# Optimization experiments

Measured on AMD Instinct MI355X. Metric: run time of the kernel, lower is better.

Reference implementation:

```python
import jax, jax.numpy as jnp
import numpy as np

N_HEADS = 12
WINDOW = 12
STRIDE = 3
N_ANCHORS = 12
EPS = 1e-6


def fmap(x):
    # elu(x) + 1 non-negative feature map
    return jax.nn.elu(x) + 1.0


def setup_inputs() -> dict:
    key = jax.random.key(0)
    ks = jax.random.split(key, 4)
    B, S, D = 4, 2048, 768
    x = jax.random.normal(ks[0], (B, S, D), dtype=jnp.float32)
    qkv_w = jax.random.normal(ks[1], (3 * D, D), dtype=jnp.float32) * 0.02
    out_w = jax.random.normal(ks[2], (D, D), dtype=jnp.float32) * 0.02
    anchor_q = jax.random.normal(ks[3], (1, N_ANCHORS, D), dtype=jnp.float32) * 0.02
    w_local = jnp.float32(1.0 / 2.0)
    w_stride = jnp.float32(1.0 / 3.0)
    w_global = jnp.float32(1.0 / 6.0)
    return {"x": x, "qkv_w": qkv_w, "out_w": out_w, "anchor_q": anchor_q,
            "w_local": w_local, "w_stride": w_stride, "w_global": w_global}


def _local_band(q, k, v, window):
    B, H, S, D = q.shape
    w = min(window, S)
    half = w // 2
    # pad with zeros BEFORE feature map (padded keys become elu(0)+1 = 1, as in torch)
    k_pad = jnp.pad(k, ((0, 0), (0, 0), (half, half), (0, 0)))
    v_pad = jnp.pad(v, ((0, 0), (0, 0), (half, half), (0, 0)))
    q_f = fmap(q)
    k_f = fmap(k_pad)
    idx = jnp.arange(S)[:, None] + jnp.arange(w)[None, :]  # [S, w] window gather
    k_unf = k_f[:, :, idx, :]   # [B,H,S,w,D]
    v_unf = v_pad[:, :, idx, :]  # [B,H,S,w,D]
    qk = jnp.einsum('bhsd,bhswd->bhsw', q_f, k_unf)
    out = jnp.einsum('bhsw,bhswd->bhsd', qk, v_unf)
    norm = jnp.clip(qk.sum(-1, keepdims=True), 1e-6, None)
    return out / norm


def _stride_band(q, k, v, stride):
    k_s = fmap(k[:, :, ::stride])
    v_s = v[:, :, ::stride]
    q_f = fmap(q)
    kv = jnp.einsum('bhsd,bhse->bhde', k_s, v_s)
    out = jnp.einsum('bhsd,bhde->bhse', q_f, kv)
    k_sum = k_s.sum(axis=2)
    norm = jnp.clip(jnp.einsum('bhsd,bhd->bhs', q_f, k_sum)[..., None], 1e-6, None)
    return out / norm


def _global_band(q, k, v, anchor_q, n_heads, n_anchors):
    B, H, S, D = q.shape
    aq = anchor_q.reshape(1, n_heads, n_anchors, D)  # [1,H,A,hd]
    aq = jnp.broadcast_to(aq, (B, n_heads, n_anchors, D))
    aq_f = fmap(aq)
    k_f = fmap(k)
    kv = jnp.einsum('bhsd,bhse->bhde', k_f, v)
    anchor_out = jnp.einsum('bhad,bhde->bhae', aq_f, kv)
    k_sum = k_f.sum(axis=2)
    anchor_norm = jnp.clip(jnp.einsum('bhad,bhd->bha', aq_f, k_sum)[..., None], 1e-6, None)
    anchor_out = anchor_out / anchor_norm
    q_f = fmap(q)
    anchor_k = fmap(aq)
    qk = jnp.einsum('bhsd,bhad->bhsa', q_f, anchor_k)
    out = jnp.einsum('bhsa,bhae->bhse', qk, anchor_out)
    qk_sum = jnp.clip(qk.sum(-1, keepdims=True), 1e-6, None)
    return out / qk_sum


def reference(x, qkv_w, out_w, anchor_q, w_local, w_stride, w_global):
    B, S, D = x.shape
    H = N_HEADS
    hd = D // H
    qkv = (x @ qkv_w.T).reshape(B, S, 3, H, hd)
    qkv = jnp.transpose(qkv, (2, 0, 3, 1, 4))  # [3,B,H,S,hd]
    q, k, v = qkv[0], qkv[1], qkv[2]
    wn = jax.nn.softmax(jnp.stack([w_local, w_stride, w_global]))
    wl, ws, wg = wn[0], wn[1], wn[2]
    out_local = _local_band(q, k, v, WINDOW)
    out_stride = _stride_band(q, k, v, STRIDE)
    out_global = _global_band(q, k, v, anchor_q, H, N_ANCHORS)
    out = wl * out_local + ws * out_stride + wg * out_global
    out = jnp.transpose(out, (0, 2, 1, 3)).reshape(B, S, D)
    return out @ out_w.T
```

## Files before the change

### kernel.cpp

```cpp
#include <hip/hip_runtime.h>
#include <hip/hip_bf16.h>

#define B_ 4
#define S_ 2048
#define D_ 768
#define H_ 12
#define HD 64

typedef __attribute__((ext_vector_type(8))) short short8;
typedef __attribute__((ext_vector_type(4))) float f32x4;

__device__ __forceinline__ float fmapf(float x) { return x > 0.f ? x + 1.f : __expf(x); }

__device__ __forceinline__ unsigned short f2bu(float f) {
    unsigned u = __float_as_uint(f);
    u += 0x7FFFu + ((u >> 16) & 1u);
    return (unsigned short)(u >> 16);
}
__device__ __forceinline__ float bu2f(unsigned short v) {
    return __uint_as_float((unsigned)v << 16);
}

__device__ __forceinline__ void gload16(const void* g, void* l) {
    __builtin_amdgcn_global_load_lds((__attribute__((address_space(1))) void*)(size_t)g,
                                     (__attribute__((address_space(3))) void*)l, 16, 0, 0);
}

union u16x8 {
    uint4 u;
    short8 s;
    unsigned short h[8];
};

__global__ __launch_bounds__(256) void convert_all(const float* __restrict__ x,
                                                   const float* __restrict__ qkvw,
                                                   const float* __restrict__ outw,
                                                   const float* __restrict__ aq,
                                                   unsigned short* __restrict__ xb,
                                                   unsigned short* __restrict__ wb,
                                                   unsigned short* __restrict__ outwb,
                                                   unsigned short* __restrict__ aqfb_g) {
    int gid = blockIdx.x * 256 + threadIdx.x;
    const float* src;
    unsigned short* dst;
    int i4;
    if (gid < 1572864) {
        src = x; dst = xb; i4 = gid;
    } else if (gid < 1572864 + 442368) {
        src = qkvw; dst = wb; i4 = gid - 1572864;
    } else if (gid < 2162688) {
        src = outw; dst = outwb; i4 = gid - (1572864 + 442368);
    } else {
        int i = gid - 2162688;
        aqfb_g[i] = f2bu(fmapf(aq[i]));
        return;
    }
    float4 v = *(const float4*)&src[i4 * 4];
    ushort4 o;
    o.x = f2bu(v.x); o.y = f2bu(v.y); o.z = f2bu(v.z); o.w = f2bu(v.w);
    *(ushort4*)&dst[i4 * 4] = o;
}

__global__ __launch_bounds__(256) void qkv_gemm_mfma(const unsigned short* __restrict__ xb,
                                                     const unsigned short* __restrict__ wb,
                                                     unsigned short* __restrict__ qfb,
                                                     unsigned short* __restrict__ kfb,
                                                     unsigned short* __restrict__ vvb) {
    __shared__ __attribute__((aligned(16))) unsigned short shmem[18432];
    const int K = 768;
    int orig = blockIdx.x;
    int swz = (orig & 7) * 144 + (orig >> 3);
    int mt = swz / 18, nt = swz - mt * 18;
    int n0 = nt * 128, m0 = mt * 128;
    int tid = threadIdx.x, lane = tid & 63, wave = tid >> 6;
    int wm = (wave & 1) * 64, wn = (wave >> 1) * 64;
    int quad = lane >> 4, l15 = lane & 15;
    f32x4 acc[4][4];
#pragma unroll
    for (int i = 0; i < 4; i++)
#pragma unroll
        for (int j = 0; j < 4; j++) acc[i][j] = 0.f;

    const unsigned short* ga0 = xb + (size_t)(m0 + (tid >> 2)) * K + (tid & 3) * 8;
    const unsigned short* ga1 = xb + (size_t)(m0 + 64 + (tid >> 2)) * K + (tid & 3) * 8;
    const unsigned short* gb0 = wb + (size_t)(n0 + (tid >> 2)) * K + (tid & 3) * 8;
    const unsigned short* gb1 = wb + (size_t)(n0 + 64 + (tid >> 2)) * K + (tid & 3) * 8;

    auto stage = [&](int bufi, int kk) {
        gload16(ga0 + kk, shmem + bufi * 4096 + wave * 512);
        gload16(ga1 + kk, shmem + bufi * 4096 + 2048 + wave * 512);
        gload16(gb0 + kk, shmem + 8192 + bufi * 4096 + wave * 512);
        gload16(gb1 + kk, shmem + 8192 + bufi * 4096 + 2048 + wave * 512);
    };
    auto compute = [&](int bufi) {
        short8 af[4], bfr[4];
#pragma unroll
        for (int i = 0; i < 4; i++)
            af[i] = *(short8*)&shmem[bufi * 4096 + (wm + i * 16 + l15) * 32 + quad * 8];
#pragma unroll
        for (int j = 0; j < 4; j++)
            bfr[j] = *(short8*)&shmem[8192 + bufi * 4096 + (wn + j * 16 + l15) * 32 + quad * 8];
#pragma unroll
        for (int i = 0; i < 4; i++)
#pragma unroll
            for (int j = 0; j < 4; j++)
                acc[i][j] = __builtin_amdgcn_mfma_f32_16x16x32_bf16(af[i], bfr[j], acc[i][j], 0, 0, 0);
    };

    stage(0, 0);
    int buf = 0;
    for (int t = 0; t < 23; t++) {
        stage(buf ^ 1, (t + 1) * 32);
        asm volatile("s_waitcnt vmcnt(4)" ::: "memory");
        __builtin_amdgcn_s_barrier();
        __builtin_amdgcn_sched_barrier(0);
        compute(buf);
        asm volatile("" ::: "memory");
        __builtin_amdgcn_s_barrier();
        buf ^= 1;
    }
    asm volatile("s_waitcnt vmcnt(0)" ::: "memory");
    __builtin_amdgcn_s_barrier();
    __builtin_amdgcn_sched_barrier(0);
    compute(buf);

    __syncthreads();
    {
        int colbase = n0 + wn;
        int t3 = colbase / 768;
        int r = colbase - t3 * 768;
        int h = r >> 6;
        int mstart = m0 + wm;
        int bb = mstart >> 11, sstart = mstart & 2047;
        unsigned short* ldsw = shmem + wave * 4608;
#pragma unroll
        for (int j = 0; j < 4; j++)
#pragma unroll
            for (int i = 0; i < 4; i++)
#pragma unroll
                for (int rr = 0; rr < 4; rr++) {
                    float val = acc[i][j][rr];
                    unsigned short o = (t3 == 2) ? f2bu(val) : f2bu(fmapf(val));
                    ldsw[(i * 16 + quad * 4 + rr) * 72 + j * 16 + l15] = o;
                }
        unsigned short* gb = (t3 == 0 ? qfb : (t3 == 1 ? kfb : vvb)) +
                             (((size_t)(bb * H_ + h) * S_) + sstart) * (size_t)HD;
#pragma unroll
        for (int c = 0; c < 8; c++) {
            int tok = c * 8 + (lane >> 3);
            uint4 vd = *(uint4*)&ldsw[tok * 72 + (lane & 7) * 8];
            *(uint4*)&gb[(size_t)tok * 64 + (lane & 7) * 8] = vd;
        }
    }
}

__global__ __launch_bounds__(512) void band_partial(const unsigned short* __restrict__ kfb,
                                                    const unsigned short* __restrict__ vvb,
                                                    float* __restrict__ pkv,
                                                    float* __restrict__ pks) {
    int bh = blockIdx.x >> 4, chunk = blockIdx.x & 15;
    int sbase = chunk * 128;
    const unsigned short* kfp = kfb + (size_t)bh * S_ * HD + (size_t)sbase * HD;
    const unsigned short* vp = vvb + (size_t)bh * S_ * HD + (size_t)sbase * HD;
    int tid = threadIdx.x;
    int d = tid & 63, eg = tid >> 6, e0 = eg * 8;
    float accg[8], accs[8];
#pragma unroll
    for (int i = 0; i < 8; i++) { accg[i] = 0.f; accs[i] = 0.f; }
    float ksg = 0.f, kss = 0.f;
#pragma unroll 4
    for (int s = 0; s < 128; s++) {
        float kd = bu2f(kfp[(size_t)s * HD + d]);
        bool str = ((sbase + s) % 3) == 0;
        ksg += kd;
        u16x8 va;
        va.u = *(const uint4*)&vp[(size_t)s * HD + e0];
        float vf[8];
#pragma unroll
        for (int i = 0; i < 8; i++) vf[i] = bu2f(va.h[i]);
#pragma unroll
        for (int i = 0; i < 8; i++) accg[i] += kd * vf[i];
        if (str) {
            kss += kd;
#pragma unroll
            for (int i = 0; i < 8; i++) accs[i] += kd * vf[i];
        }
    }
    float* pg = pkv + (size_t)blockIdx.x * 2 * 4096;
#pragma unroll
    for (int i = 0; i < 8; i++) pg[d * 64 + e0 + i] = accg[i];
#pragma unroll
    for (int i = 0; i < 8; i++) pg[4096 + d * 64 + e0 + i] = accs[i];
    if (eg == 0) {
        pks[blockIdx.x * 128 + d] = ksg;
        pks[blockIdx.x * 128 + 64 + d] = kss;
    }
}

__global__ __launch_bounds__(256) void band_reduce(const float* __restrict__ pkv,
                                                   const float* __restrict__ pks,
                                                   const float* __restrict__ aq,
                                                   unsigned short* __restrict__ kvsTb,
                                                   unsigned short* __restrict__ ksumsb,
                                                   unsigned short* __restrict__ aoutTb) {
    int bh = blockIdx.x >> 2, eb = blockIdx.x & 3, e0 = eb * 16;
    int h = bh % H_;
    __shared__ float kvgL[64][17];
    __shared__ float ksgL[64];
    __shared__ float anorm[12];
    int tid = threadIdx.x;
    for (int idx = tid; idx < 1024; idx += 256) {
        int d = idx >> 4, j = idx & 15;
        float sg = 0.f, ss = 0.f;
        const float* p = pkv + (size_t)(bh * 16) * 2 * 4096 + d * 64 + e0 + j;
#pragma unroll 4
        for (int c = 0; c < 16; c++) {
            sg += p[0];
            ss += p[4096];
            p += 2 * 4096;
        }
        kvgL[d][j] = sg;
        kvsTb[(size_t)bh * 4096 + (e0 + j) * 64 + d] = f2bu(ss);
    }
    if (tid < 64) {
        float sg = 0.f, ss = 0.f;
#pragma unroll 4
        for (int c = 0; c < 16; c++) {
            sg += pks[(bh * 16 + c) * 128 + tid];
            ss += pks[(bh * 16 + c) * 128 + 64 + tid];
        }
        ksgL[tid] = sg;
        if (eb == 0) ksumsb[bh * 64 + tid] = f2bu(ss);
    }
    __syncthreads();
    if (tid < 12) {
        float nrm = 0.f;
        for (int dd = 0; dd < 64; dd++)
            nrm += fmapf(aq[h * 768 + tid * 64 + dd]) * ksgL[dd];
        anorm[tid] = fmaxf(nrm, 1e-6f);
    }
    __syncthreads();
    if (tid < 192) {
        int a = tid >> 4, j = tid & 15;
        float acc = 0.f;
        for (int dd = 0; dd < 64; dd++)
            acc += fmapf(aq[h * 768 + a * 64 + dd]) * kvgL[dd][j];
        aoutTb[(size_t)bh * 768 + (e0 + j) * 12 + a] = f2bu(acc / anorm[a]);
    }
}

__global__ __launch_bounds__(256) void combine(const unsigned short* __restrict__ qfb,
                                               const unsigned short* __restrict__ kfb,
                                               const unsigned short* __restrict__ vvb,
                                               const unsigned short* __restrict__ aqfb_g,
                                               const unsigned short* __restrict__ kvsTb,
                                               const unsigned short* __restrict__ ksumsb,
                                               const unsigned short* __restrict__ aoutTb,
                                               const float* __restrict__ wlp,
                                               const float* __restrict__ wsp,
                                               const float* __restrict__ wgp,
                                               unsigned short* __restrict__ attnb) {
    __shared__ __attribute__((aligned(16))) unsigned short aqfb[16][72];
    __shared__ __attribute__((aligned(16))) unsigned short vtbT[64][104];
    __shared__ __attribute__((aligned(16))) unsigned short plb[64][104];
    __shared__ __attribute__((aligned(16))) unsigned short qkgb[64][40];
    __shared__ float nrm[4][3][16];
    int bh = blockIdx.x >> 5, stile = blockIdx.x & 31;
    int b = bh / H_, h = bh % H_;
    int s0 = stile * 64;
    int tid = threadIdx.x, lane = tid & 63, wave = tid >> 6;
    int quad = lane >> 4, l15 = lane & 15;
    const unsigned short* qfp = qfb + (size_t)bh * S_ * HD;
    const unsigned short* kfp = kfb + (size_t)bh * S_ * HD;
    const unsigned short* vp = vvb + (size_t)bh * S_ * HD;
    float a0 = wlp[0], a1 = wsp[0], a2 = wgp[0];
    float mx = fmaxf(a0, fmaxf(a1, a2));
    float ew0 = __expf(a0 - mx), ew1 = __expf(a1 - mx), ew2 = __expf(a2 - mx);
    float inv = 1.f / (ew0 + ew1 + ew2);
    float wl = ew0 * inv, wsb = ew1 * inv, wg = ew2 * inv;
    for (int i = tid; i < 96 * 64; i += 256) {
        int k = i >> 6, e = i & 63;
        int gs = s0 + k - 6;
        unsigned short v_ = (k < 75 && gs >= 0 && gs < S_) ? vp[(size_t)gs * HD + e]
                                                           : (unsigned short)0;
        vtbT[e][k] = v_;
    }
    if (tid < 192) {
        int a = tid >> 4, c = (tid & 15) * 4;
        *(ushort4*)&aqfb[a][c] = *(const ushort4*)&aqfb_g[h * 768 + a * 64 + c];
    }
    if (tid < 64) aqfb[12][tid] = ksumsb[bh * 64 + tid];
    if (tid < 192) aqfb[13 + (tid >> 6)][tid & 63] = 0;
    for (int i = tid; i < 1024; i += 256) {
        plb[i >> 4][80 + (i & 15)] = 0;
        qkgb[i >> 4][16 + (i & 15)] = 0;
    }
    __syncthreads();
    u16x8 qa0, qa1;
    {
        const unsigned short* qr = qfp + (size_t)(s0 + wave * 16 + l15) * HD + quad * 8;
        qa0.u = *(const uint4*)qr;
        qa1.u = *(const uint4*)(qr + 32);
    }
#pragma unroll
    for (int tj = 0; tj < 5; tj++) {
        int row = tj * 16 + l15;
        int gs = s0 + row - 6;
        bool valid = (row < 75) && (gs >= 0) && (gs < S_);
        int gsc = gs < 0 ? 0 : (gs > S_ - 1 ? S_ - 1 : gs);
        const unsigned short* kr = kfp + (size_t)gsc * HD + quad * 8;
        u16x8 b0, b1, ones;
        ones.u = make_uint4(0x3F803F80u, 0x3F803F80u, 0x3F803F80u, 0x3F803F80u);
        b0.u = *(const uint4*)kr;
        b1.u = *(const uint4*)(kr + 32);
        if (!valid) { b0 = ones; b1 = ones; }
        f32x4 c = {0.f, 0.f, 0.f, 0.f};
        c = __builtin_amdgcn_mfma_f32_16x16x32_bf16(qa0.s, b0.s, c, 0, 0, 0);
        c = __builtin_amdgcn_mfma_f32_16x16x32_bf16(qa1.s, b1.s, c, 0, 0, 0);
        int col = tj * 16 + l15;
#pragma unroll
        for (int rr = 0; rr < 4; rr++) {
            int tok = wave * 16 + quad * 4 + rr;
            int which = col - tok;
            plb[tok][col] = (which >= 0 && which < 12) ? f2bu(c[rr]) : (unsigned short)0;
        }
    }
    {
        f32x4 c = {0.f, 0.f, 0.f, 0.f};
        short8 bfr0 = *(short8*)&aqfb[l15][quad * 8];
        short8 bfr1 = *(short8*)&aqfb[l15][32 + quad * 8];
        c = __builtin_amdgcn_mfma_f32_16x16x32_bf16(qa0.s, bfr0, c, 0, 0, 0);
        c = __builtin_amdgcn_mfma_f32_16x16x32_bf16(qa1.s, bfr1, c, 0, 0, 0);
#pragma unroll
        for (int rr = 0; rr < 4; rr++) qkgb[wave * 16 + quad * 4 + rr][l15] = f2bu(c[rr]);
    }
    if (lane < 16) {
        int t = wave * 16 + lane;
        float sl = 0.f;
#pragma unroll
        for (int j = 0; j < 12; j++) sl += bu2f(plb[t][t + j]);
        float sg = 0.f;
#pragma unroll
        for (int a = 0; a < 12; a++) sg += bu2f(qkgb[t][a]);
        nrm[wave][0][lane] = wl / fmaxf(sl, 1e-6f);
        nrm[wave][1][lane] = wg / fmaxf(sg, 1e-6f);
        nrm[wave][2][lane] = wsb / fmaxf(bu2f(qkgb[t][12]), 1e-6f);
    }
#pragma unroll
    for (int j2 = 0; j2 < 4; j2++) {
        int e = j2 * 16 + l15;
        f32x4 cL = {0.f, 0.f, 0.f, 0.f};
        f32x4 cG = {0.f, 0.f, 0.f, 0.f};
        f32x4 cS = {0.f, 0.f, 0.f, 0.f};
#pragma unroll
        for (int kk = 0; kk < 3; kk++) {
            short8 afr = *(short8*)&plb[wave * 16 + l15][kk * 32 + quad * 8];
            short8 bfr = *(short8*)&vtbT[e][kk * 32 + quad * 8];
            cL = __builtin_amdgcn_mfma_f32_16x16x32_bf16(afr, bfr, cL, 0, 0, 0);
        }
        {
            short8 afr = *(short8*)&qkgb[wave * 16 + l15][quad * 8];
            u16x8 bo;
            bo.u = make_uint4(0u, 0u, 0u, 0u);
            const unsigned* ap = (const unsigned*)(aoutTb + (size_t)bh * 768 + e * 12);
            if (quad == 0) {
                bo.u.x = ap[0]; bo.u.y = ap[1]; bo.u.z = ap[2]; bo.u.w = ap[3];
            } else if (quad == 1) {
                bo.u.x = ap[4]; bo.u.y = ap[5];
            }
            cG = __builtin_amdgcn_mfma_f32_16x16x32_bf16(afr, bo.s, cG, 0, 0, 0);
        }
        {
            const unsigned short* kvp = kvsTb + (size_t)bh * 4096 + e * 64 + quad * 8;
            u16x8 bk0, bk1;
            bk0.u = *(const uint4*)kvp;
            bk1.u = *(const uint4*)(kvp + 32);
            cS = __builtin_amdgcn_mfma_f32_16x16x32_bf16(qa0.s, bk0.s, cS, 0, 0, 0);
            cS = __builtin_amdgcn_mfma_f32_16x16x32_bf16(qa1.s, bk1.s, cS, 0, 0, 0);
        }
#pragma unroll
        for (int rr = 0; rr < 4; rr++) {
            int tq = quad * 4 + rr;
            int tok = wave * 16 + tq;
            float res = cL[rr] * nrm[wave][0][tq] + cS[rr] * nrm[wave][2][tq] +
                        cG[rr] * nrm[wave][1][tq];
            attnb[((size_t)(b * S_ + s0 + tok)) * 768 + h * 64 + e] = f2bu(res);
        }
    }
}

__global__ __launch_bounds__(256) void out_gemm_mfma(const unsigned short* __restrict__ attnb,
                                                     const unsigned short* __restrict__ wb,
                                                     float* __restrict__ out) {
    __shared__ __attribute__((aligned(16))) unsigned short As[2][128 * 32];
    __shared__ __attribute__((aligned(16))) unsigned short Bs[2][128 * 32];
    const int K = 768;
    int orig = blockIdx.x;
    int swz = (orig & 7) * 48 + (orig >> 3);
    int mt = swz / 6, nt = swz - mt * 6;
    int n0 = nt * 128, m0 = mt * 128;
    int tid = threadIdx.x, lane = tid & 63, wave = tid >> 6;
    int wm = (wave & 1) * 64, wn = (wave >> 1) * 64;
    int quad = lane >> 4, l15 = lane & 15;
    f32x4 acc[4][4];
#pragma unroll
    for (int i = 0; i < 4; i++)
#pragma unroll
        for (int j = 0; j < 4; j++) acc[i][j] = 0.f;

    const unsigned short* ga0 = attnb + (size_t)(m0 + (tid >> 2)) * K + (tid & 3) * 8;
    const unsigned short* ga1 = attnb + (size_t)(m0 + 64 + (tid >> 2)) * K + (tid & 3) * 8;
    const unsigned short* gb0 = wb + (size_t)(n0 + (tid >> 2)) * K + (tid & 3) * 8;
    const unsigned short* gb1 = wb + (size_t)(n0 + 64 + (tid >> 2)) * K + (tid & 3) * 8;

    auto stage = [&](int bufi, int kk) {
        gload16(ga0 + kk, &As[bufi][wave * 512]);
        gload16(ga1 + kk, &As[bufi][2048 + wave * 512]);
        gload16(gb0 + kk, &Bs[bufi][wave * 512]);
        gload16(gb1 + kk, &Bs[bufi][2048 + wave * 512]);
    };
    auto compute = [&](int bufi) {
        short8 af[4], bfr[4];
#pragma unroll
        for (int i = 0; i < 4; i++)
            af[i] = *(short8*)&As[bufi][(wm + i * 16 + l15) * 32 + quad * 8];
#pragma unroll
        for (int j = 0; j < 4; j++)
            bfr[j] = *(short8*)&Bs[bufi][(wn + j * 16 + l15) * 32 + quad * 8];
#pragma unroll
        for (int i = 0; i < 4; i++)
#pragma unroll
            for (int j = 0; j < 4; j++)
                acc[i][j] = __builtin_amdgcn_mfma_f32_16x16x32_bf16(af[i], bfr[j], acc[i][j], 0, 0, 0);
    };

    stage(0, 0);
    int buf = 0;
    for (int t = 0; t < 23; t++) {
        stage(buf ^ 1, (t + 1) * 32);
        asm volatile("s_waitcnt vmcnt(4)" ::: "memory");
        __builtin_amdgcn_s_barrier();
        __builtin_amdgcn_sched_barrier(0);
        compute(buf);
        asm volatile("" ::: "memory");
        __builtin_amdgcn_s_barrier();
        buf ^= 1;
    }
    asm volatile("s_waitcnt vmcnt(0)" ::: "memory");
    __builtin_amdgcn_s_barrier();
    __builtin_amdgcn_sched_barrier(0);
    compute(buf);

#pragma unroll
    for (int j = 0; j < 4; j++) {
        int col = n0 + wn + j * 16 + l15;
#pragma unroll
        for (int i = 0; i < 4; i++) {
#pragma unroll
            for (int rr = 0; rr < 4; rr++) {
                int m = m0 + wm + i * 16 + quad * 4 + rr;
                out[(size_t)m * 768 + col] = acc[i][j][rr];
            }
        }
    }
}

extern "C" void kernel_launch(void* const* d_in, const int* in_sizes, int n_in,
                              void* d_out, int out_size, void* d_ws, size_t ws_size,
                              hipStream_t stream) {
    const float* x = (const float*)d_in[0];
    const float* qkvw = (const float*)d_in[1];
    const float* outw = (const float*)d_in[2];
    const float* aq = (const float*)d_in[3];
    const float* wlp = (const float*)d_in[4];
    const float* wsp = (const float*)d_in[5];
    const float* wgp = (const float*)d_in[6];

    float* ws = (float*)d_ws;
    const size_t NBH = (size_t)B_ * H_ * S_ * HD;
    unsigned short* qfb = (unsigned short*)ws;
    unsigned short* kfb = (unsigned short*)(ws + NBH / 2);
    unsigned short* vvb = (unsigned short*)(ws + NBH);
    float* attn_region = ws + 2 * NBH;
    unsigned short* xb = (unsigned short*)attn_region;
    unsigned short* wb = (unsigned short*)(attn_region + 3145728);
    float* pkv = attn_region;
    unsigned short* attnb = (unsigned short*)attn_region;
    unsigned short* kvsTb = (unsigned short*)(attn_region + NBH);
    unsigned short* ksumsb = kvsTb + 48 * 4096;
    unsigned short* aoutTb = ksumsb + 48 * 64;
    unsigned short* aqfb_g = aoutTb + 48 * 768;
    float* pks = attn_region + NBH + 122880;
    unsigned short* outwb = (unsigned short*)(pks + 768 * 128);

    convert_all<<<8484, 256, 0, stream>>>(x, qkvw, outw, aq, xb, wb, outwb, aqfb_g);
    qkv_gemm_mfma<<<1152, 256, 0, stream>>>(xb, wb, qfb, kfb, vvb);
    band_partial<<<48 * 16, 512, 0, stream>>>(kfb, vvb, pkv, pks);
    band_reduce<<<48 * 4, 256, 0, stream>>>(pkv, pks, aq, kvsTb, ksumsb, aoutTb);
    combine<<<48 * 32, 256, 0, stream>>>(qfb, kfb, vvb, aqfb_g, kvsTb, ksumsb, aoutTb,
                                         wlp, wsp, wgp, attnb);
    out_gemm_mfma<<<384, 256, 0, stream>>>(attnb, outwb, (float*)d_out);
}
```

Baseline: 254.7 us.

## Emit transposed K/V from QKV GEMM and use MFMA for band partial sums

The QKV GEMM epilogue now also writes K (feature-mapped) and V in a transposed [d][s] layout. band_partial uses these with bf16 MFMA, applying a stride mask and a ones-vector product for the key sums, in place of scalar FMA loops. combine loads the V window with vectorized loads from the transposed layout, with the window offset shifted to keep 8-element alignment. This costs extra epilogue writes for K and a larger workspace footprint.

```diff
diff --git a/kernel.cpp b/kernel.cpp
--- a/kernel.cpp
+++ b/kernel.cpp
@@ -65,7 +65,8 @@
                                                      const unsigned short* __restrict__ wb,
                                                      unsigned short* __restrict__ qfb,
                                                      unsigned short* __restrict__ kfb,
-                                                     unsigned short* __restrict__ vvb) {
+                                                     unsigned short* __restrict__ kTb,
+                                                     unsigned short* __restrict__ vTb) {
     __shared__ __attribute__((aligned(16))) unsigned short shmem[18432];
     const int K = 768;
     int orig = blockIdx.x;
@@ -133,67 +134,104 @@
         int mstart = m0 + wm;
         int bb = mstart >> 11, sstart = mstart & 2047;
         unsigned short* ldsw = shmem + wave * 4608;
-#pragma unroll
-        for (int j = 0; j < 4; j++)
-#pragma unroll
-            for (int i = 0; i < 4; i++)
-#pragma unroll
-                for (int rr = 0; rr < 4; rr++) {
-                    float val = acc[i][j][rr];
-                    unsigned short o = (t3 == 2) ? f2bu(val) : f2bu(fmapf(val));
-                    ldsw[(i * 16 + quad * 4 + rr) * 72 + j * 16 + l15] = o;
-                }
-        unsigned short* gb = (t3 == 0 ? qfb : (t3 == 1 ? kfb : vvb)) +
-                             (((size_t)(bb * H_ + h) * S_) + sstart) * (size_t)HD;
-#pragma unroll
-        for (int c = 0; c < 8; c++) {
-            int tok = c * 8 + (lane >> 3);
-            uint4 vd = *(uint4*)&ldsw[tok * 72 + (lane & 7) * 8];
-            *(uint4*)&gb[(size_t)tok * 64 + (lane & 7) * 8] = vd;
-        }
-    }
-}
-
-__global__ __launch_bounds__(512) void band_partial(const unsigned short* __restrict__ kfb,
-                                                    const unsigned short* __restrict__ vvb,
+        if (t3 <= 1) {
+#pragma unroll
+            for (int j = 0; j < 4; j++)
+#pragma unroll
+                for (int i = 0; i < 4; i++)
+#pragma unroll
+                    for (int rr = 0; rr < 4; rr++) {
+                        float val = acc[i][j][rr];
+                        ldsw[(i * 16 + quad * 4 + rr) * 72 + j * 16 + l15] = f2bu(fmapf(val));
+                    }
+            unsigned short* gbp = (t3 == 0 ? qfb : kfb) +
+                                  (((size_t)(bb * H_ + h) * S_) + sstart) * (size_t)HD;
+#pragma unroll
+            for (int c = 0; c < 8; c++) {
+                int tok = c * 8 + (lane >> 3);
+                uint4 vd = *(uint4*)&ldsw[tok * 72 + (lane & 7) * 8];
+                *(uint4*)&gbp[(size_t)tok * 64 + (lane & 7) * 8] = vd;
+            }
+        }
+        if (t3 >= 1) {
+#pragma unroll
+            for (int j = 0; j < 4; j++)
+#pragma unroll
+                for (int i = 0; i < 4; i++)
+#pragma unroll
+                    for (int rr = 0; rr < 4; rr++) {
+                        float val = acc[i][j][rr];
+                        unsigned short o = (t3 == 1) ? f2bu(fmapf(val)) : f2bu(val);
+                        ldsw[(j * 16 + l15) * 72 + i * 16 + quad * 4 + rr] = o;
+                    }
+            unsigned short* gt = (t3 == 1 ? kTb : vTb) +
+                                 ((size_t)(bb * H_ + h) * 64) * (size_t)S_ + sstart;
+#pragma unroll
+            for (int c = 0; c < 8; c++) {
+                int d = c * 8 + (lane >> 3);
+                uint4 vd = *(uint4*)&ldsw[d * 72 + (lane & 7) * 8];
+                *(uint4*)&gt[(size_t)d * S_ + (lane & 7) * 8] = vd;
+            }
+        }
+    }
+}
+
+__global__ __launch_bounds__(256) void band_partial(const unsigned short* __restrict__ kTb,
+                                                    const unsigned short* __restrict__ vTb,
                                                     float* __restrict__ pkv,
                                                     float* __restrict__ pks) {
     int bh = blockIdx.x >> 4, chunk = blockIdx.x & 15;
-    int sbase = chunk * 128;
-    const unsigned short* kfp = kfb + (size_t)bh * S_ * HD + (size_t)sbase * HD;
-    const unsigned short* vp = vvb + (size_t)bh * S_ * HD + (size_t)sbase * HD;
-    int tid = threadIdx.x;
-    int d = tid & 63, eg = tid >> 6, e0 = eg * 8;
-    float accg[8], accs[8];
-#pragma unroll
-    for (int i = 0; i < 8; i++) { accg[i] = 0.f; accs[i] = 0.f; }
-    float ksg = 0.f, kss = 0.f;
-#pragma unroll 4
-    for (int s = 0; s < 128; s++) {
-        float kd = bu2f(kfp[(size_t)s * HD + d]);
-        bool str = ((sbase + s) % 3) == 0;
-        ksg += kd;
-        u16x8 va;
-        va.u = *(const uint4*)&vp[(size_t)s * HD + e0];
-        float vf[8];
-#pragma unroll
-        for (int i = 0; i < 8; i++) vf[i] = bu2f(va.h[i]);
-#pragma unroll
-        for (int i = 0; i < 8; i++) accg[i] += kd * vf[i];
-        if (str) {
-            kss += kd;
-#pragma unroll
-            for (int i = 0; i < 8; i++) accs[i] += kd * vf[i];
+    int s0 = chunk * 128;
+    int tid = threadIdx.x, lane = tid & 63, wave = tid >> 6;
+    int quad = lane >> 4, l15 = lane & 15;
+    const unsigned short* kT = kTb + (size_t)bh * 64 * S_;
+    const unsigned short* vT = vTb + (size_t)bh * 64 * S_;
+    f32x4 cg[4], cs[4], og, os;
+#pragma unroll
+    for (int j = 0; j < 4; j++) { cg[j] = 0.f; cs[j] = 0.f; }
+    og = 0.f; os = 0.f;
+    u16x8 ONES;
+    ONES.u = make_uint4(0x3F803F80u, 0x3F803F80u, 0x3F803F80u, 0x3F803F80u);
+    const uint4 M0 = make_uint4(0x0000FFFFu, 0xFFFF0000u, 0u, 0x0000FFFFu);
+    const uint4 M1 = make_uint4(0u, 0x0000FFFFu, 0xFFFF0000u, 0u);
+    const uint4 M2 = make_uint4(0xFFFF0000u, 0u, 0x0000FFFFu, 0xFFFF0000u);
+#pragma unroll
+    for (int st = 0; st < 4; st++) {
+        int sb = s0 + st * 32 + quad * 8;
+        u16x8 A;
+        A.u = *(const uint4*)&kT[(size_t)(wave * 16 + l15) * S_ + sb];
+        int rmod = sb % 3;
+        uint4 m = (rmod == 0) ? M0 : ((rmod == 1) ? M1 : M2);
+        u16x8 Am;
+        Am.u.x = A.u.x & m.x; Am.u.y = A.u.y & m.y;
+        Am.u.z = A.u.z & m.z; Am.u.w = A.u.w & m.w;
+        og = __builtin_amdgcn_mfma_f32_16x16x32_bf16(A.s, ONES.s, og, 0, 0, 0);
+        os = __builtin_amdgcn_mfma_f32_16x16x32_bf16(Am.s, ONES.s, os, 0, 0, 0);
+#pragma unroll
+        for (int j = 0; j < 4; j++) {
+            u16x8 Bf;
+            Bf.u = *(const uint4*)&vT[(size_t)(j * 16 + l15) * S_ + sb];
+            cg[j] = __builtin_amdgcn_mfma_f32_16x16x32_bf16(A.s, Bf.s, cg[j], 0, 0, 0);
+            cs[j] = __builtin_amdgcn_mfma_f32_16x16x32_bf16(Am.s, Bf.s, cs[j], 0, 0, 0);
         }
     }
     float* pg = pkv + (size_t)blockIdx.x * 2 * 4096;
 #pragma unroll
-    for (int i = 0; i < 8; i++) pg[d * 64 + e0 + i] = accg[i];
-#pragma unroll
-    for (int i = 0; i < 8; i++) pg[4096 + d * 64 + e0 + i] = accs[i];
-    if (eg == 0) {
-        pks[blockIdx.x * 128 + d] = ksg;
-        pks[blockIdx.x * 128 + 64 + d] = kss;
+    for (int j = 0; j < 4; j++)
+#pragma unroll
+        for (int rr = 0; rr < 4; rr++) {
+            int d = wave * 16 + quad * 4 + rr;
+            int e = j * 16 + l15;
+            pg[d * 64 + e] = cg[j][rr];
+            pg[4096 + d * 64 + e] = cs[j][rr];
+        }
+    if (l15 == 0) {
+#pragma unroll
+        for (int rr = 0; rr < 4; rr++) {
+            int d = wave * 16 + quad * 4 + rr;
+            pks[blockIdx.x * 128 + d] = og[rr];
+            pks[blockIdx.x * 128 + 64 + d] = os[rr];
+        }
     }
 }
 
@@ -251,7 +289,7 @@
 
 __global__ __launch_bounds__(256) void combine(const unsigned short* __restrict__ qfb,
                                                const unsigned short* __restrict__ kfb,
-                                               const unsigned short* __restrict__ vvb,
+                                               const unsigned short* __restrict__ vTb,
                                                const unsigned short* __restrict__ aqfb_g,
                                                const unsigned short* __restrict__ kvsTb,
                                                const unsigned short* __restrict__ ksumsb,
@@ -272,18 +310,26 @@
     int quad = lane >> 4, l15 = lane & 15;
     const unsigned short* qfp = qfb + (size_t)bh * S_ * HD;
     const unsigned short* kfp = kfb + (size_t)bh * S_ * HD;
-    const unsigned short* vp = vvb + (size_t)bh * S_ * HD;
+    const unsigned short* vTp = vTb + (size_t)bh * 64 * S_;
     float a0 = wlp[0], a1 = wsp[0], a2 = wgp[0];
     float mx = fmaxf(a0, fmaxf(a1, a2));
     float ew0 = __expf(a0 - mx), ew1 = __expf(a1 - mx), ew2 = __expf(a2 - mx);
     float inv = 1.f / (ew0 + ew1 + ew2);
     float wl = ew0 * inv, wsb = ew1 * inv, wg = ew2 * inv;
-    for (int i = tid; i < 96 * 64; i += 256) {
-        int k = i >> 6, e = i & 63;
-        int gs = s0 + k - 6;
-        unsigned short v_ = (k < 75 && gs >= 0 && gs < S_) ? vp[(size_t)gs * HD + e]
-                                                           : (unsigned short)0;
-        vtbT[e][k] = v_;
+    for (int u = tid; u < 64 * 12; u += 256) {
+        int e = u & 63, c = u >> 6;
+        int k0 = c * 8;
+        int gs0 = s0 - 8 + k0;
+        const unsigned short* src = vTp + (size_t)e * S_ + gs0;
+        if (gs0 >= 0 && gs0 + 8 <= S_) {
+            *(uint4*)&vtbT[e][k0] = *(const uint4*)src;
+        } else {
+#pragma unroll
+            for (int i = 0; i < 8; i++) {
+                int gs = gs0 + i;
+                vtbT[e][k0 + i] = (gs >= 0 && gs < S_) ? src[i] : (unsigned short)0;
+            }
+        }
     }
     if (tid < 192) {
         int a = tid >> 4, c = (tid & 15) * 4;
@@ -305,8 +351,8 @@
 #pragma unroll
     for (int tj = 0; tj < 5; tj++) {
         int row = tj * 16 + l15;
-        int gs = s0 + row - 6;
-        bool valid = (row < 75) && (gs >= 0) && (gs < S_);
+        int gs = s0 + row - 8;
+        bool valid = (row < 78) && (gs >= 0) && (gs < S_);
         int gsc = gs < 0 ? 0 : (gs > S_ - 1 ? S_ - 1 : gs);
         const unsigned short* kr = kfp + (size_t)gsc * HD + quad * 8;
         u16x8 b0, b1, ones;
@@ -322,7 +368,7 @@
         for (int rr = 0; rr < 4; rr++) {
             int tok = wave * 16 + quad * 4 + rr;
             int which = col - tok;
-            plb[tok][col] = (which >= 0 && which < 12) ? f2bu(c[rr]) : (unsigned short)0;
+            plb[tok][col] = (which >= 2 && which < 14) ? f2bu(c[rr]) : (unsigned short)0;
         }
     }
     {
@@ -338,7 +384,7 @@
         int t = wave * 16 + lane;
         float sl = 0.f;
 #pragma unroll
-        for (int j = 0; j < 12; j++) sl += bu2f(plb[t][t + j]);
+        for (int j = 0; j < 12; j++) sl += bu2f(plb[t][t + 2 + j]);
         float sg = 0.f;
 #pragma unroll
         for (int a = 0; a < 12; a++) sg += bu2f(qkgb[t][a]);
@@ -479,8 +525,9 @@
     float* ws = (float*)d_ws;
     const size_t NBH = (size_t)B_ * H_ * S_ * HD;
     unsigned short* qfb = (unsigned short*)ws;
-    unsigned short* kfb = (unsigned short*)(ws + NBH / 2);
-    unsigned short* vvb = (unsigned short*)(ws + NBH);
+    unsigned short* kfb = qfb + NBH;
+    unsigned short* kTb = kfb + NBH;
+    unsigned short* vTb = kTb + NBH;
     float* attn_region = ws + 2 * NBH;
     unsigned short* xb = (unsigned short*)attn_region;
     unsigned short* wb = (unsigned short*)(attn_region + 3145728);
@@ -494,10 +541,10 @@
     unsigned short* outwb = (unsigned short*)(pks + 768 * 128);
 
     convert_all<<<8484, 256, 0, stream>>>(x, qkvw, outw, aq, xb, wb, outwb, aqfb_g);
-    qkv_gemm_mfma<<<1152, 256, 0, stream>>>(xb, wb, qfb, kfb, vvb);
-    band_partial<<<48 * 16, 512, 0, stream>>>(kfb, vvb, pkv, pks);
+    qkv_gemm_mfma<<<1152, 256, 0, stream>>>(xb, wb, qfb, kfb, kTb, vTb);
+    band_partial<<<48 * 16, 256, 0, stream>>>(kTb, vTb, pkv, pks);
     band_reduce<<<48 * 4, 256, 0, stream>>>(pkv, pks, aq, kvsTb, ksumsb, aoutTb);
-    combine<<<48 * 32, 256, 0, stream>>>(qfb, kfb, vvb, aqfb_g, kvsTb, ksumsb, aoutTb,
+    combine<<<48 * 32, 256, 0, stream>>>(qfb, kfb, vTb, aqfb_g, kvsTb, ksumsb, aoutTb,
                                          wlp, wsp, wgp, attnb);
     out_gemm_mfma<<<384, 256, 0, stream>>>(attnb, outwb, (float*)d_out);
 }
```

Measured after the change: 218.5 us. -14.2%, faster.
